# Kernel optimization log

Measured on AMD Instinct MI355X. Metric: run time of the kernel, lower is better.

## Reference

```python
import jax, jax.numpy as jnp
import numpy as np

C_IN = 256
C_RED = max(4, C_IN // 4)  # 64


def setup_inputs() -> dict:
    key = jax.random.key(0)
    k1, k2, k3, k4, k5 = jax.random.split(key, 5)
    B, C, H, W = 4, C_IN, 64, 64
    x = jax.random.normal(k1, (B, C, H, W), dtype=jnp.float32)
    # 1x1 convs (no bias) are just channel matmuls: weight shape (out_ch, in_ch)
    s_in = 1.0 / np.sqrt(C)
    s_red = 1.0 / np.sqrt(C_RED)
    Wq = jax.random.normal(k2, (C_RED, C), dtype=jnp.float32) * s_in
    Wk = jax.random.normal(k3, (C_RED, C), dtype=jnp.float32) * s_in
    Wv = jax.random.normal(k4, (C_RED, C), dtype=jnp.float32) * s_in
    Wp = jax.random.normal(k5, (C, C_RED), dtype=jnp.float32) * s_red
    return {"x": x, "Wq": Wq, "Wk": Wk, "Wv": Wv, "Wp": Wp}


def reference(x, Wq, Wk, Wv, Wp):
    B, C, H, W = x.shape
    N = H * W
    xf = x.reshape(B, C, N)                       # (B, C, N)
    q = jnp.einsum('rc,bcn->bnr', Wq, xf)         # (B, N, c_red)
    k = jnp.einsum('rc,bcn->brn', Wk, xf)         # (B, c_red, N)
    v = jnp.einsum('rc,bcn->bnr', Wv, xf)         # (B, N, c_red)
    scale = 1.0 / jnp.sqrt(jnp.float32(k.shape[1]))
    attn = jnp.einsum('bnr,brm->bnm', q, k) * scale   # (B, N, N)
    attn = jax.nn.softmax(attn, axis=-1)
    out = jnp.einsum('bnm,bmr->brn', attn, v)     # (B, c_red, N)
    out = jnp.einsum('cr,brn->bcn', Wp, out)      # (B, C, N)
    return out.reshape(B, C, H, W) + x
```

## Files before the change

### kernel.cpp

```cpp
#include <hip/hip_runtime.h>
#include <hip/hip_bf16.h>

#define CIN 256
#define CRED 64
#define NB 4
#define NN 4096

typedef float v4f __attribute__((ext_vector_type(4)));
typedef short v8s __attribute__((ext_vector_type(8)));
typedef unsigned short u16;
typedef u16 u16x4 __attribute__((ext_vector_type(4)));
typedef u16 u16x8 __attribute__((ext_vector_type(8)));
typedef unsigned int u32;

#define LOG2E 1.4426950408889634f

__device__ __forceinline__ u16 f2bf(float f) {
    union { float f; u32 u; } v; v.f = f;
    u32 r = (v.u + 0x7FFFu + ((v.u >> 16) & 1u)) >> 16;
    return (u16)r;
}
__device__ __forceinline__ float bf2f(u16 s) {
    union { u32 u; float f; } v; v.u = ((u32)s) << 16;
    return v.f;
}
__device__ __forceinline__ u32 pkbf(float a, float b) {
    float2 f; f.x = a; f.y = b;
    __hip_bfloat162 h = __float22bfloat162_rn(f);
    union { __hip_bfloat162 h; u32 u; } c; c.h = h;
    return c.u;
}
__device__ __forceinline__ v4f mfma16(v8s a, v8s b, v4f c) {
    return __builtin_amdgcn_mfma_f32_16x16x32_bf16(a, b, c, 0, 0, 0);
}
__device__ __forceinline__ float fexp2(float x) {
#if __has_builtin(__builtin_amdgcn_exp2f)
    return __builtin_amdgcn_exp2f(x);
#else
    return exp2f(x);
#endif
}

__global__ __launch_bounds__(256) void k_wconv(const float* __restrict__ Wq,
                                               const float* __restrict__ Wk,
                                               const float* __restrict__ Wv,
                                               const float* __restrict__ Wp,
                                               u16* __restrict__ Wb,
                                               u16* __restrict__ WpB) {
    int t = threadIdx.x;
    if (blockIdx.x < 48) {
        int idx = (blockIdx.x * 256 + t) * 4;
        int row = idx >> 8;
        int mat = row >> 6, r = row & 63, col = idx & 255;
        const float* src = (mat == 0) ? Wq : (mat == 1) ? Wk : Wv;
        float4 v = *(const float4*)&src[r * 256 + col];
        float s = (mat == 0) ? (0.125f * LOG2E) : 1.0f;
        u16x4 o;
        o[0] = f2bf(v.x * s); o[1] = f2bf(v.y * s);
        o[2] = f2bf(v.z * s); o[3] = f2bf(v.w * s);
        *(u16x4*)&Wb[idx] = o;
    } else {
        int idx = ((blockIdx.x - 48) * 256 + t) * 4;
        float4 v = *(const float4*)&Wp[idx];
        u16x4 o;
        o[0] = f2bf(v.x); o[1] = f2bf(v.y);
        o[2] = f2bf(v.z); o[3] = f2bf(v.w);
        *(u16x4*)&WpB[idx] = o;
    }
}

__global__ __launch_bounds__(256) void k_qkvm(const float* __restrict__ x,
                                              const u16* __restrict__ Wb,
                                              u16* __restrict__ Q, u16* __restrict__ K,
                                              u16* __restrict__ V) {
    int t = threadIdx.x;
    int wv = t >> 6, lane = t & 63, c15 = lane & 15, quad = lane >> 4;
    int n0g = blockIdx.x * 32;
    int b = n0g >> 12, nb = n0g & 4095;
    const float* xb = x + ((size_t)b << 20);

    v8s Af[2][8];
#pragma unroll
    for (int nt = 0; nt < 2; ++nt) {
        const float* px = xb + nb + nt * 16 + c15 + (size_t)quad * 8 * 4096;
#pragma unroll
        for (int kc = 0; kc < 8; ++kc) {
            float f[8];
#pragma unroll
            for (int j = 0; j < 8; ++j)
                f[j] = px[((size_t)kc * 32 + j) * 4096];
            union { v8s s; u32 w[4]; } pk;
            pk.w[0] = pkbf(f[0], f[1]); pk.w[1] = pkbf(f[2], f[3]);
            pk.w[2] = pkbf(f[4], f[5]); pk.w[3] = pkbf(f[6], f[7]);
            Af[nt][kc] = pk.s;
        }
    }

#pragma unroll
    for (int rti = 0; rti < 3; ++rti) {
        int rt = wv * 3 + rti;
        const u16* wrow = Wb + (size_t)(rt * 16 + c15) * 256 + quad * 8;
        v8s Bf[8];
#pragma unroll
        for (int kc = 0; kc < 8; ++kc) Bf[kc] = *(const v8s*)&wrow[kc * 32];
#pragma unroll
        for (int nt = 0; nt < 2; ++nt) {
            v4f acc = {0.f, 0.f, 0.f, 0.f};
#pragma unroll
            for (int kc = 0; kc < 8; ++kc)
                acc = mfma16(Af[nt][kc], Bf[kc], acc);
            if (rt < 8) {
                u16* base = (rt < 4) ? Q : K;
                u16* dst = base + ((size_t)b << 18)
                         + (size_t)(nb + nt * 16 + quad * 4) * 64
                         + (rt & 3) * 16 + c15;
#pragma unroll
                for (int g = 0; g < 4; ++g) dst[g * 64] = f2bf(acc[g]);
            } else {
                int hi2 = ((nb + nt * 16) >> 4) & 3;
                size_t base = ((size_t)b * 64 + (rt - 8) * 16 + c15) * 4096
                            + (size_t)((nb + nt * 16) & ~63) + hi2;
#pragma unroll
                for (int g = 0; g < 4; ++g)
                    V[base + (quad * 4 + g) * 4] = f2bf(acc[g]);
            }
        }
    }
}

__global__ __launch_bounds__(256, 4) void k_flash(const u16* __restrict__ Q,
                                                  const u16* __restrict__ K,
                                                  const u16* __restrict__ V,
                                                  u16* __restrict__ OP,
                                                  float* __restrict__ Lb,
                                                  int sh) {
    __shared__ u16 Kl[64][72];
    __shared__ u16 Vl[64][72];
    __shared__ u16 Pl[4][32][72];
    int t = threadIdx.x;
    int p = blockIdx.x & ((1u << sh) - 1);
    int tile = blockIdx.x >> sh;
    int b = tile >> 5;
    int n0 = (tile & 31) * 128;
    int wv = t >> 6;
    int lane = t & 63;
    int c15 = lane & 15;
    int quad = lane >> 4;
    int nw = n0 + wv * 32;
    const u16* Qb = Q + (size_t)b * NN * 64;
    const u16* Kb = K + (size_t)b * NN * 64;
    const u16* Vb = V + (size_t)b * 64 * NN;

    v8s Qa[2][2];
#pragma unroll
    for (int rg = 0; rg < 2; ++rg)
#pragma unroll
        for (int c2 = 0; c2 < 2; ++c2)
            Qa[rg][c2] = *(const v8s*)&Qb[(size_t)(nw + rg * 16 + c15) * 64 + c2 * 32 + quad * 8];

    v4f O[2][4];
    float ls[2][4];
#pragma unroll
    for (int rg = 0; rg < 2; ++rg)
#pragma unroll
        for (int g = 0; g < 4; ++g) {
            ls[rg][g] = 0.f;
#pragma unroll
            for (int cg = 0; cg < 4; ++cg) O[rg][cg][g] = 0.f;
        }

    int mlen = NN >> sh;
    int m0 = p * mlen;
    int iters = mlen >> 6;
    int srow = t >> 3, scol = (t & 7) * 8;

    v8s kpre[2], vpre[2];
#pragma unroll
    for (int pass = 0; pass < 2; ++pass) {
        int rr = srow + pass * 32;
        kpre[pass] = *(const v8s*)&Kb[(size_t)(m0 + rr) * 64 + scol];
        vpre[pass] = *(const v8s*)&Vb[(size_t)rr * NN + m0 + scol];
    }

    for (int it = 0; it < iters; ++it) {
#pragma unroll
        for (int pass = 0; pass < 2; ++pass) {
            int rr = srow + pass * 32;
            *(v8s*)&Kl[rr][scol] = kpre[pass];
            *(v8s*)&Vl[rr][scol] = vpre[pass];
        }
        __syncthreads();

        if (it + 1 < iters) {
            int mt = m0 + (it + 1) * 64;
#pragma unroll
            for (int pass = 0; pass < 2; ++pass) {
                int rr = srow + pass * 32;
                kpre[pass] = *(const v8s*)&Kb[(size_t)(mt + rr) * 64 + scol];
                vpre[pass] = *(const v8s*)&Vb[(size_t)rr * NN + mt + scol];
            }
        }

        v4f S[2][4];
#pragma unroll
        for (int rg = 0; rg < 2; ++rg)
#pragma unroll
            for (int s = 0; s < 4; ++s)
#pragma unroll
                for (int g = 0; g < 4; ++g) S[rg][s][g] = 0.f;
#pragma unroll
        for (int s = 0; s < 4; ++s)
#pragma unroll
            for (int c2 = 0; c2 < 2; ++c2) {
                v8s kb = *(const v8s*)&Kl[s * 16 + c15][c2 * 32 + quad * 8];
                S[0][s] = mfma16(Qa[0][c2], kb, S[0][s]);
                S[1][s] = mfma16(Qa[1][c2], kb, S[1][s]);
            }

#pragma unroll
        for (int rg = 0; rg < 2; ++rg) {
            float E[4][4];
#pragma unroll
            for (int s = 0; s < 4; ++s)
#pragma unroll
                for (int g = 0; g < 4; ++g) {
                    float e = fexp2(S[rg][s][g]);
                    E[s][g] = e;
                    ls[rg][g] += e;
                }
#pragma unroll
            for (int g = 0; g < 4; ++g) {
                union { u16x4 v; u32 w[2]; } p2;
                p2.w[0] = pkbf(E[0][g], E[1][g]);
                p2.w[1] = pkbf(E[2][g], E[3][g]);
                *(u16x4*)&Pl[wv][rg * 16 + quad * 4 + g][c15 * 4] = p2.v;
            }
        }

        v8s Pa[2][2];
#pragma unroll
        for (int rg = 0; rg < 2; ++rg)
#pragma unroll
            for (int c2 = 0; c2 < 2; ++c2)
                Pa[rg][c2] = *(const v8s*)&Pl[wv][rg * 16 + c15][c2 * 32 + quad * 8];
#pragma unroll
        for (int cg = 0; cg < 4; ++cg)
#pragma unroll
            for (int c2 = 0; c2 < 2; ++c2) {
                v8s vb = *(const v8s*)&Vl[cg * 16 + c15][c2 * 32 + quad * 8];
                O[0][cg] = mfma16(Pa[0][c2], vb, O[0][cg]);
                O[1][cg] = mfma16(Pa[1][c2], vb, O[1][cg]);
            }
        __syncthreads();
    }

    u16* OPp = OP + (size_t)p * (NB * NN * 64) + (size_t)b * NN * 64;
#pragma unroll
    for (int rg = 0; rg < 2; ++rg)
#pragma unroll
        for (int cg = 0; cg < 4; ++cg)
#pragma unroll
            for (int g = 0; g < 4; ++g) {
                int n = nw + rg * 16 + quad * 4 + g;
                OPp[(size_t)n * 64 + cg * 16 + c15] = f2bf(O[rg][cg][g]);
            }
#pragma unroll
    for (int rg = 0; rg < 2; ++rg)
#pragma unroll
        for (int g = 0; g < 4; ++g) {
            float v = ls[rg][g];
#pragma unroll
            for (int off = 1; off <= 8; off <<= 1) v += __shfl_xor(v, off);
            ls[rg][g] = v;
        }
    if (c15 == 0) {
        float* Lp = Lb + (size_t)p * (NB * NN) + (size_t)b * NN;
#pragma unroll
        for (int rg = 0; rg < 2; ++rg)
#pragma unroll
            for (int g = 0; g < 4; ++g) {
                int n = nw + rg * 16 + quad * 4 + g;
                Lp[n] = ls[rg][g];
            }
    }
}

#define OMP 72
__global__ __launch_bounds__(256) void k_proj(const u16* __restrict__ OP,
                                              const float* __restrict__ Lb,
                                              const u16* __restrict__ WpB,
                                              const float* __restrict__ x,
                                              float* __restrict__ out,
                                              int nsp) {
    __shared__ u16 Om[16 * OMP];
    int t = threadIdx.x;
    int b = blockIdx.x >> 8;
    int n0 = (blockIdx.x & 255) * 16;

    {
        int n_l = t >> 4, r0 = (t & 15) * 4;
        size_t nidx = (size_t)b * NN + n0 + n_l;
        float o[4] = {0.f, 0.f, 0.f, 0.f};
        float l = 0.f;
        for (int p = 0; p < nsp; ++p) {
            u16x4 u = *(const u16x4*)&OP[((size_t)p * (NB * NN) + nidx) * 64 + r0];
#pragma unroll
            for (int j = 0; j < 4; ++j) o[j] += bf2f(u[j]);
            l += Lb[(size_t)p * (NB * NN) + nidx];
        }
        float inv = 1.0f / l;
        union { u16x4 v; u32 w[2]; } p2;
        p2.w[0] = pkbf(o[0] * inv, o[1] * inv);
        p2.w[1] = pkbf(o[2] * inv, o[3] * inv);
        *(u16x4*)&Om[n_l * OMP + r0] = p2.v;
    }
    __syncthreads();

    int lane = t & 63, wvv = t >> 6, c15 = lane & 15, quad = lane >> 4;
    v8s B0 = *(const v8s*)&Om[c15 * OMP + quad * 8];
    v8s B1 = *(const v8s*)&Om[c15 * OMP + 32 + quad * 8];
#pragma unroll
    for (int ct0 = 0; ct0 < 4; ++ct0) {
        int ct = wvv * 4 + ct0;
        const u16* wrow = WpB + (size_t)(ct * 16 + c15) * 64 + quad * 8;
        v8s A0 = *(const v8s*)&wrow[0];
        v8s A1 = *(const v8s*)&wrow[32];
        v4f acc = {0.f, 0.f, 0.f, 0.f};
        acc = mfma16(A0, B0, acc);
        acc = mfma16(A1, B1, acc);
        size_t base = ((size_t)(b * 256 + ct * 16 + quad * 4)) * 4096 + n0 + c15;
#pragma unroll
        for (int g = 0; g < 4; ++g)
            out[base + (size_t)g * 4096] = acc[g] + x[base + (size_t)g * 4096];
    }
}

extern "C" void kernel_launch(void* const* d_in, const int* in_sizes, int n_in,
                              void* d_out, int out_size, void* d_ws, size_t ws_size,
                              hipStream_t stream) {
    const float* x  = (const float*)d_in[0];
    const float* Wq = (const float*)d_in[1];
    const float* Wk = (const float*)d_in[2];
    const float* Wv = (const float*)d_in[3];
    const float* Wp = (const float*)d_in[4];
    float* out = (float*)d_out;
    char* ws = (char*)d_ws;

    int nsp = (ws_size >= (size_t)24 * 1024 * 1024) ? 8 : 4;
    int sh = (nsp == 8) ? 3 : 2;

    u16* Wb  = (u16*)(ws);
    u16* WpB = (u16*)(ws + 131072);
    u16* Q   = (u16*)(ws + 262144);
    u16* K   = (u16*)(ws + 262144 + 2097152);
    u16* V   = (u16*)(ws + 262144 + 2 * 2097152);
    u16* OP  = (u16*)(ws + 262144 + 3 * 2097152);
    float* Lbuf = (float*)(ws + 262144 + (size_t)(3 + nsp) * 2097152);

    k_wconv<<<64, 256, 0, stream>>>(Wq, Wk, Wv, Wp, Wb, WpB);
    k_qkvm<<<512, 256, 0, stream>>>(x, Wb, Q, K, V);
    k_flash<<<NB * 32 * nsp, 256, 0, stream>>>(Q, K, V, OP, Lbuf, sh);
    k_proj<<<NB * 256, 256, 0, stream>>>(OP, Lbuf, WpB, x, out, nsp);
}
```

Measured before the change: 126.1 us.

## Fold weight conversion into consumers, split QKV grid, double-buffer K/V in LDS

Removes the separate weight-conversion kernel: the QKV and projection kernels now read fp32 weights and convert them to bf16 inline. The QKV kernel grid is tripled so each block computes only one of Q, K or V, which means each block reloads and reconverts its x tile. The flash kernel double-buffers K/V in shared memory so there is one barrier per iteration instead of two, and its launch bound drops from 4 to 2 waves per SIMD. The aim is to cut one launch plus a barrier, at the cost of three times the x reads and possibly lower occupancy.

Measured after the change: 136.1 us. +7.9%, slower.

```diff
diff --git a/kernel.cpp b/kernel.cpp
--- a/kernel.cpp
+++ b/kernel.cpp
@@ -41,43 +41,21 @@
 #endif
 }
 
-__global__ __launch_bounds__(256) void k_wconv(const float* __restrict__ Wq,
-                                               const float* __restrict__ Wk,
-                                               const float* __restrict__ Wv,
-                                               const float* __restrict__ Wp,
-                                               u16* __restrict__ Wb,
-                                               u16* __restrict__ WpB) {
-    int t = threadIdx.x;
-    if (blockIdx.x < 48) {
-        int idx = (blockIdx.x * 256 + t) * 4;
-        int row = idx >> 8;
-        int mat = row >> 6, r = row & 63, col = idx & 255;
-        const float* src = (mat == 0) ? Wq : (mat == 1) ? Wk : Wv;
-        float4 v = *(const float4*)&src[r * 256 + col];
-        float s = (mat == 0) ? (0.125f * LOG2E) : 1.0f;
-        u16x4 o;
-        o[0] = f2bf(v.x * s); o[1] = f2bf(v.y * s);
-        o[2] = f2bf(v.z * s); o[3] = f2bf(v.w * s);
-        *(u16x4*)&Wb[idx] = o;
-    } else {
-        int idx = ((blockIdx.x - 48) * 256 + t) * 4;
-        float4 v = *(const float4*)&Wp[idx];
-        u16x4 o;
-        o[0] = f2bf(v.x); o[1] = f2bf(v.y);
-        o[2] = f2bf(v.z); o[3] = f2bf(v.w);
-        *(u16x4*)&WpB[idx] = o;
-    }
-}
-
 __global__ __launch_bounds__(256) void k_qkvm(const float* __restrict__ x,
-                                              const u16* __restrict__ Wb,
+                                              const float* __restrict__ Wq,
+                                              const float* __restrict__ Wk,
+                                              const float* __restrict__ Wv,
                                               u16* __restrict__ Q, u16* __restrict__ K,
                                               u16* __restrict__ V) {
     int t = threadIdx.x;
     int wv = t >> 6, lane = t & 63, c15 = lane & 15, quad = lane >> 4;
-    int n0g = blockIdx.x * 32;
-    int b = n0g >> 12, nb = n0g & 4095;
+    int mat = blockIdx.x >> 9;
+    int sub = blockIdx.x & 511;
+    int b = sub >> 7;
+    int nb = (sub & 127) * 32;
     const float* xb = x + ((size_t)b << 20);
+    const float* W = (mat == 0) ? Wq : (mat == 1) ? Wk : Wv;
+    float s = (mat == 0) ? (0.125f * LOG2E) : 1.0f;
 
     v8s Af[2][8];
 #pragma unroll
@@ -96,46 +74,52 @@
         }
     }
 
-#pragma unroll
-    for (int rti = 0; rti < 3; ++rti) {
-        int rt = wv * 3 + rti;
-        const u16* wrow = Wb + (size_t)(rt * 16 + c15) * 256 + quad * 8;
-        v8s Bf[8];
-#pragma unroll
-        for (int kc = 0; kc < 8; ++kc) Bf[kc] = *(const v8s*)&wrow[kc * 32];
-#pragma unroll
-        for (int nt = 0; nt < 2; ++nt) {
-            v4f acc = {0.f, 0.f, 0.f, 0.f};
-#pragma unroll
-            for (int kc = 0; kc < 8; ++kc)
-                acc = mfma16(Af[nt][kc], Bf[kc], acc);
-            if (rt < 8) {
-                u16* base = (rt < 4) ? Q : K;
-                u16* dst = base + ((size_t)b << 18)
-                         + (size_t)(nb + nt * 16 + quad * 4) * 64
-                         + (rt & 3) * 16 + c15;
-#pragma unroll
-                for (int g = 0; g < 4; ++g) dst[g * 64] = f2bf(acc[g]);
-            } else {
-                int hi2 = ((nb + nt * 16) >> 4) & 3;
-                size_t base = ((size_t)b * 64 + (rt - 8) * 16 + c15) * 4096
-                            + (size_t)((nb + nt * 16) & ~63) + hi2;
-#pragma unroll
-                for (int g = 0; g < 4; ++g)
-                    V[base + (quad * 4 + g) * 4] = f2bf(acc[g]);
-            }
-        }
-    }
-}
-
-__global__ __launch_bounds__(256, 4) void k_flash(const u16* __restrict__ Q,
+    v8s Bf[8];
+    {
+        const float* wr = W + (size_t)(wv * 16 + c15) * 256 + quad * 8;
+#pragma unroll
+        for (int kc = 0; kc < 8; ++kc) {
+            float4 a = *(const float4*)&wr[kc * 32];
+            float4 c = *(const float4*)&wr[kc * 32 + 4];
+            union { v8s s; u32 w[4]; } pk;
+            pk.w[0] = pkbf(a.x * s, a.y * s); pk.w[1] = pkbf(a.z * s, a.w * s);
+            pk.w[2] = pkbf(c.x * s, c.y * s); pk.w[3] = pkbf(c.z * s, c.w * s);
+            Bf[kc] = pk.s;
+        }
+    }
+
+#pragma unroll
+    for (int nt = 0; nt < 2; ++nt) {
+        v4f acc = {0.f, 0.f, 0.f, 0.f};
+#pragma unroll
+        for (int kc = 0; kc < 8; ++kc)
+            acc = mfma16(Af[nt][kc], Bf[kc], acc);
+        if (mat < 2) {
+            u16* base = (mat == 0) ? Q : K;
+            u16* dst = base + ((size_t)b << 18)
+                     + (size_t)(nb + nt * 16 + quad * 4) * 64
+                     + wv * 16 + c15;
+#pragma unroll
+            for (int g = 0; g < 4; ++g) dst[g * 64] = f2bf(acc[g]);
+        } else {
+            int hi2 = ((nb + nt * 16) >> 4) & 3;
+            size_t base = ((size_t)b * 64 + wv * 16 + c15) * 4096
+                        + (size_t)((nb + nt * 16) & ~63) + hi2;
+#pragma unroll
+            for (int g = 0; g < 4; ++g)
+                V[base + (quad * 4 + g) * 4] = f2bf(acc[g]);
+        }
+    }
+}
+
+__global__ __launch_bounds__(256, 2) void k_flash(const u16* __restrict__ Q,
                                                   const u16* __restrict__ K,
                                                   const u16* __restrict__ V,
                                                   u16* __restrict__ OP,
                                                   float* __restrict__ Lb,
                                                   int sh) {
-    __shared__ u16 Kl[64][72];
-    __shared__ u16 Vl[64][72];
+    __shared__ u16 Kl[2][64][72];
+    __shared__ u16 Vl[2][64][72];
     __shared__ u16 Pl[4][32][72];
     int t = threadIdx.x;
     int p = blockIdx.x & ((1u << sh) - 1);
@@ -174,30 +158,25 @@
     int iters = mlen >> 6;
     int srow = t >> 3, scol = (t & 7) * 8;
 
-    v8s kpre[2], vpre[2];
 #pragma unroll
     for (int pass = 0; pass < 2; ++pass) {
         int rr = srow + pass * 32;
-        kpre[pass] = *(const v8s*)&Kb[(size_t)(m0 + rr) * 64 + scol];
-        vpre[pass] = *(const v8s*)&Vb[(size_t)rr * NN + m0 + scol];
-    }
+        *(v8s*)&Kl[0][rr][scol] = *(const v8s*)&Kb[(size_t)(m0 + rr) * 64 + scol];
+        *(v8s*)&Vl[0][rr][scol] = *(const v8s*)&Vb[(size_t)rr * NN + m0 + scol];
+    }
+    __syncthreads();
 
     for (int it = 0; it < iters; ++it) {
-#pragma unroll
-        for (int pass = 0; pass < 2; ++pass) {
-            int rr = srow + pass * 32;
-            *(v8s*)&Kl[rr][scol] = kpre[pass];
-            *(v8s*)&Vl[rr][scol] = vpre[pass];
-        }
-        __syncthreads();
-
+        int cur = it & 1, nxt = cur ^ 1;
+
+        v8s kn[2], vn[2];
         if (it + 1 < iters) {
             int mt = m0 + (it + 1) * 64;
 #pragma unroll
             for (int pass = 0; pass < 2; ++pass) {
                 int rr = srow + pass * 32;
-                kpre[pass] = *(const v8s*)&Kb[(size_t)(mt + rr) * 64 + scol];
-                vpre[pass] = *(const v8s*)&Vb[(size_t)rr * NN + mt + scol];
+                kn[pass] = *(const v8s*)&Kb[(size_t)(mt + rr) * 64 + scol];
+                vn[pass] = *(const v8s*)&Vb[(size_t)rr * NN + mt + scol];
             }
         }
 
@@ -212,7 +191,7 @@
         for (int s = 0; s < 4; ++s)
 #pragma unroll
             for (int c2 = 0; c2 < 2; ++c2) {
-                v8s kb = *(const v8s*)&Kl[s * 16 + c15][c2 * 32 + quad * 8];
+                v8s kb = *(const v8s*)&Kl[cur][s * 16 + c15][c2 * 32 + quad * 8];
                 S[0][s] = mfma16(Qa[0][c2], kb, S[0][s]);
                 S[1][s] = mfma16(Qa[1][c2], kb, S[1][s]);
             }
@@ -247,10 +226,19 @@
         for (int cg = 0; cg < 4; ++cg)
 #pragma unroll
             for (int c2 = 0; c2 < 2; ++c2) {
-                v8s vb = *(const v8s*)&Vl[cg * 16 + c15][c2 * 32 + quad * 8];
+                v8s vb = *(const v8s*)&Vl[cur][cg * 16 + c15][c2 * 32 + quad * 8];
                 O[0][cg] = mfma16(Pa[0][c2], vb, O[0][cg]);
                 O[1][cg] = mfma16(Pa[1][c2], vb, O[1][cg]);
             }
+
+        if (it + 1 < iters) {
+#pragma unroll
+            for (int pass = 0; pass < 2; ++pass) {
+                int rr = srow + pass * 32;
+                *(v8s*)&Kl[nxt][rr][scol] = kn[pass];
+                *(v8s*)&Vl[nxt][rr][scol] = vn[pass];
+            }
+        }
         __syncthreads();
     }
 
@@ -288,7 +276,7 @@
 #define OMP 72
 __global__ __launch_bounds__(256) void k_proj(const u16* __restrict__ OP,
                                               const float* __restrict__ Lb,
-                                              const u16* __restrict__ WpB,
+                                              const float* __restrict__ Wp,
                                               const float* __restrict__ x,
                                               float* __restrict__ out,
                                               int nsp) {
@@ -322,12 +310,19 @@
 #pragma unroll
     for (int ct0 = 0; ct0 < 4; ++ct0) {
         int ct = wvv * 4 + ct0;
-        const u16* wrow = WpB + (size_t)(ct * 16 + c15) * 64 + quad * 8;
-        v8s A0 = *(const v8s*)&wrow[0];
-        v8s A1 = *(const v8s*)&wrow[32];
+        const float* wr = Wp + (size_t)(ct * 16 + c15) * 64 + quad * 8;
+        float4 wa = *(const float4*)&wr[0];
+        float4 wb = *(const float4*)&wr[4];
+        float4 wc = *(const float4*)&wr[32];
+        float4 wd = *(const float4*)&wr[36];
+        union { v8s s; u32 w[4]; } pa, pb;
+        pa.w[0] = pkbf(wa.x, wa.y); pa.w[1] = pkbf(wa.z, wa.w);
+        pa.w[2] = pkbf(wb.x, wb.y); pa.w[3] = pkbf(wb.z, wb.w);
+        pb.w[0] = pkbf(wc.x, wc.y); pb.w[1] = pkbf(wc.z, wc.w);
+        pb.w[2] = pkbf(wd.x, wd.y); pb.w[3] = pkbf(wd.z, wd.w);
         v4f acc = {0.f, 0.f, 0.f, 0.f};
-        acc = mfma16(A0, B0, acc);
-        acc = mfma16(A1, B1, acc);
+        acc = mfma16(pa.s, B0, acc);
+        acc = mfma16(pb.s, B1, acc);
         size_t base = ((size_t)(b * 256 + ct * 16 + quad * 4)) * 4096 + n0 + c15;
 #pragma unroll
         for (int g = 0; g < 4; ++g)
@@ -349,16 +344,13 @@
     int nsp = (ws_size >= (size_t)24 * 1024 * 1024) ? 8 : 4;
     int sh = (nsp == 8) ? 3 : 2;
 
-    u16* Wb  = (u16*)(ws);
-    u16* WpB = (u16*)(ws + 131072);
-    u16* Q   = (u16*)(ws + 262144);
-    u16* K   = (u16*)(ws + 262144 + 2097152);
-    u16* V   = (u16*)(ws + 262144 + 2 * 2097152);
-    u16* OP  = (u16*)(ws + 262144 + 3 * 2097152);
-    float* Lbuf = (float*)(ws + 262144 + (size_t)(3 + nsp) * 2097152);
-
-    k_wconv<<<64, 256, 0, stream>>>(Wq, Wk, Wv, Wp, Wb, WpB);
-    k_qkvm<<<512, 256, 0, stream>>>(x, Wb, Q, K, V);
+    u16* Q   = (u16*)(ws);
+    u16* K   = (u16*)(ws + 2097152);
+    u16* V   = (u16*)(ws + 2 * 2097152);
+    u16* OP  = (u16*)(ws + 3 * 2097152);
+    float* Lbuf = (float*)(ws + (size_t)(3 + nsp) * 2097152);
+
+    k_qkvm<<<1536, 256, 0, stream>>>(x, Wq, Wk, Wv, Q, K, V);
     k_flash<<<NB * 32 * nsp, 256, 0, stream>>>(Q, K, V, OP, Lbuf, sh);
-    k_proj<<<NB * 256, 256, 0, stream>>>(OP, Lbuf, WpB, x, out, nsp);
-}
+    k_proj<<<NB * 256, 256, 0, stream>>>(OP, Lbuf, Wp, x, out, nsp);
+}
```
